# Performance work log

Measured on AMD Instinct MI355X. Metric: run time of the kernel, lower is better.

Reference implementation:

```python
import jax, jax.numpy as jnp
import numpy as np

D_MODEL = 2048
N_HEADS = 16
D_HEAD = D_MODEL // N_HEADS  # 128
T_MAX = 2048
B, T = 2, 2048


def _build_rope_cache(T_max, d_head):
    pos = jnp.arange(T_max, dtype=jnp.float32)[:, None]
    dim = jnp.arange(0, d_head, 2, dtype=jnp.float32)
    freqs = 1.0 / (10000.0 ** (dim / d_head))
    angles = pos * freqs  # [T_max, d_head//2]
    return jnp.cos(angles), jnp.sin(angles)


def _apply_rope(x, cos, sin):
    # x: [B, H, T, D]; cos/sin: [T_max, D//2]
    d2 = x.shape[-1] // 2
    x1, x2 = x[..., :d2], x[..., d2:]
    c = cos[: x.shape[2]][None, None]  # [1,1,T,D//2]
    s = sin[: x.shape[2]][None, None]
    return jnp.concatenate([x1 * c - x2 * s, x2 * c + x1 * s], axis=-1)


def setup_inputs() -> dict:
    key = jax.random.key(0)
    k1, k2, k3, k4 = jax.random.split(key, 4)
    x = jax.random.normal(k1, (B, T, D_MODEL), dtype=jnp.float32)
    Wqkv = jax.random.normal(k2, (3 * D_MODEL, D_MODEL), dtype=jnp.float32) * (D_MODEL ** -0.5)
    Wproj = jax.random.normal(k3, (D_MODEL, D_MODEL), dtype=jnp.float32) * (D_MODEL ** -0.5)
    q_gain = jnp.full((N_HEADS,), 1.0, dtype=jnp.float32) + 0.1 * jax.random.normal(k4, (N_HEADS,), dtype=jnp.float32)
    rope_cos, rope_sin = _build_rope_cache(T_MAX, D_HEAD)
    return {"x": x, "Wqkv": Wqkv, "Wproj": Wproj, "q_gain": q_gain,
            "rope_cos": rope_cos, "rope_sin": rope_sin}


def reference(x, Wqkv, Wproj, q_gain, rope_cos, rope_sin):
    Bx, Tx, C = x.shape
    H, D = N_HEADS, C // N_HEADS
    qkv = jnp.einsum('btc,fc->btf', x, Wqkv)  # [B,T,3C]
    q, k, v = jnp.split(qkv, 3, axis=2)
    q = q.reshape(Bx, Tx, H, D).transpose(0, 2, 1, 3)  # [B,H,T,D]
    k = k.reshape(Bx, Tx, H, D).transpose(0, 2, 1, 3)
    v = v.reshape(Bx, Tx, H, D).transpose(0, 2, 1, 3)
    q = _apply_rope(q, rope_cos, rope_sin)
    k = _apply_rope(k, rope_cos, rope_sin)
    q = q * q_gain[None, :, None, None]
    scale = 1.0 / jnp.sqrt(jnp.asarray(D, dtype=x.dtype))
    scores = jnp.einsum('bhqd,bhkd->bhqk', q, k) * scale
    causal = jnp.tril(jnp.ones((Tx, Tx), dtype=bool))
    scores = jnp.where(causal[None, None], scores, jnp.asarray(-jnp.inf, dtype=scores.dtype))
    attn = jax.nn.softmax(scores, axis=-1)
    y = jnp.einsum('bhqk,bhkd->bhqd', attn, v)  # [B,H,T,D]
    y = y.transpose(0, 2, 1, 3).reshape(Bx, Tx, C)
    return jnp.einsum('btc,oc->bto', y, Wproj)
```

## Files before the change

kernel.cpp:

```cpp
#include <hip/hip_runtime.h>
#include <stdint.h>

#define BB    2
#define T_SEQ 2048
#define NH    16
#define DH    128
#define DM    2048

typedef unsigned short u16;
typedef unsigned int   u32;
typedef __attribute__((ext_vector_type(8))) short short8;
typedef __attribute__((ext_vector_type(4))) short short4_t;
typedef __attribute__((ext_vector_type(4))) float floatx4;

__device__ __forceinline__ float bf2f(u16 b) { return __uint_as_float(((u32)b) << 16); }
__device__ __forceinline__ u16 f2bf(float f) {
    u32 u = __float_as_uint(f);
    u32 r = u + 0x7fffu + ((u >> 16) & 1u);
    return (u16)(r >> 16);
}

__device__ __forceinline__ short8 cvt8(const float* p) {
    floatx4 a = *(const floatx4*)p;
    floatx4 b = *(const floatx4*)(p + 4);
    short8 r;
    r[0] = (short)f2bf(a[0]); r[1] = (short)f2bf(a[1]);
    r[2] = (short)f2bf(a[2]); r[3] = (short)f2bf(a[3]);
    r[4] = (short)f2bf(b[0]); r[5] = (short)f2bf(b[1]);
    r[6] = (short)f2bf(b[2]); r[7] = (short)f2bf(b[3]);
    return r;
}

__device__ __forceinline__ void gl2lds16(const u16* g, u16* l) {
    __builtin_amdgcn_global_load_lds(
        (const __attribute__((address_space(1))) void*)g,
        (__attribute__((address_space(3))) void*)l, 16, 0, 0);
}

__global__ void detect_dtype(const u16* __restrict__ w, int* __restrict__ flag) {
    __shared__ int cnt;
    if (threadIdx.x == 0) cnt = 0;
    __syncthreads();
    int c = 0;
    for (int i = threadIdx.x; i < 2048; i += 256) {
        float v = bf2f(w[i]);
        if (!(fabsf(v) <= 1.0f)) c++;
    }
    atomicAdd(&cnt, c);
    __syncthreads();
    if (threadIdx.x == 0) *flag = (cnt > 64) ? 1 : 0;
}

__global__ void sentinel_k(const int* __restrict__ flag, float* __restrict__ out, int n) {
    if (*flag != 0) return;
    for (int i = threadIdx.x; i < n; i += 256) out[i] = (i == 0) ? 200.0f : 0.0f;
}

__global__ void fill_const(float* __restrict__ out, int n, float v0) {
    int i = blockIdx.x * 256 + threadIdx.x;
    if (i < n) out[i] = (i == 0) ? v0 : 0.0f;
}

__global__ __launch_bounds__(256) void cvt_f32_bf16(const float* __restrict__ src,
                                                    u16* __restrict__ dst, int n4,
                                                    const int* __restrict__ flag) {
    if (*flag == 0) return;
    int i = blockIdx.x * 256 + threadIdx.x;
    if (i < n4) {
        floatx4 v = ((const floatx4*)src)[i];
        short4_t r;
        r[0] = (short)f2bf(v[0]); r[1] = (short)f2bf(v[1]);
        r[2] = (short)f2bf(v[2]); r[3] = (short)f2bf(v[3]);
        ((short4_t*)dst)[i] = r;
    }
}

template<int PERM, int OF32>
__global__ __launch_bounds__(256) void gemm97(const u16* __restrict__ A,
                                              const u16* __restrict__ B,
                                              void* __restrict__ Cv,
                                              const int* __restrict__ flag,
                                              int M, int N, int K)
{
    if (*flag == 0) return;

    __shared__ __align__(16) u16 As[128 * 32];
    __shared__ __align__(16) u16 Bs[128 * 32];

    u16*   C16 = (u16*)Cv;
    float* C32 = (float*)Cv;

    const int tid  = threadIdx.x;
    const int lane = tid & 63;
    const int quad = lane >> 4;
    const int l15  = lane & 15;
    const int wave = tid >> 6;
    const int wy   = (wave >> 1) * 64;
    const int wx   = (wave & 1) * 64;
    const int rowA0 = blockIdx.y * 128;
    const int rowB0 = blockIdx.x * 128;

    const int lrow = lane >> 2;
    const int lcol = (lane & 3) << 3;
    const int segA0 = wave * 2, segA1 = wave * 2 + 1;

    const u16* gA0 = A + (size_t)(rowA0 + segA0 * 16 + lrow) * K + lcol;
    const u16* gA1 = A + (size_t)(rowA0 + segA1 * 16 + lrow) * K + lcol;
    const u16* gB0 = B + (size_t)(rowB0 + segA0 * 16 + lrow) * K + lcol;
    const u16* gB1 = B + (size_t)(rowB0 + segA1 * 16 + lrow) * K + lcol;
    u16* lA0 = &As[segA0 * 16 * 32];
    u16* lA1 = &As[segA1 * 16 * 32];
    u16* lB0 = &Bs[segA0 * 16 * 32];
    u16* lB1 = &Bs[segA1 * 16 * 32];

    floatx4 acc[4][4];
#pragma unroll
    for (int i = 0; i < 4; ++i)
#pragma unroll
        for (int j = 0; j < 4; ++j) acc[i][j] = (floatx4){0.f, 0.f, 0.f, 0.f};

    for (int k0 = 0; k0 < K; k0 += 32) {
        __syncthreads();
        gl2lds16(gA0 + k0, lA0);
        gl2lds16(gA1 + k0, lA1);
        gl2lds16(gB0 + k0, lB0);
        gl2lds16(gB1 + k0, lB1);
        __syncthreads();

        short8 a[4], b[4];
#pragma unroll
        for (int i = 0; i < 4; ++i)
            a[i] = *(const short8*)&As[(wy + i * 16 + l15) * 32 + quad * 8];
#pragma unroll
        for (int i = 0; i < 4; ++i)
            b[i] = *(const short8*)&Bs[(wx + i * 16 + l15) * 32 + quad * 8];
#pragma unroll
        for (int i = 0; i < 4; ++i)
#pragma unroll
            for (int j = 0; j < 4; ++j)
                acc[i][j] = __builtin_amdgcn_mfma_f32_16x16x32_bf16(a[i], b[j], acc[i][j], 0, 0, 0);
    }

#pragma unroll
    for (int i = 0; i < 4; ++i) {
#pragma unroll
        for (int j = 0; j < 4; ++j) {
#pragma unroll
            for (int r = 0; r < 4; ++r) {
                int row = rowA0 + wy + i * 16 + quad * 4 + r;
                int col = rowB0 + wx + j * 16 + l15;
                if (PERM == 3) {
                    int slice = rowB0 >> 11;
                    u16* dbuf = C16 + (size_t)slice * 8388608;
                    int b_ = row >> 11, t_ = row & 2047;
                    int colm = col & 2047;
                    int h_ = colm >> 7, d_ = colm & 127;
                    size_t dst;
                    if (slice < 2) {
                        dst = ((size_t)((b_ * NH + h_) * T_SEQ + t_)) * DH + d_;
                    } else {
                        int u  = t_ & 63;
                        int tp = (t_ & ~63) + ((u & 15) * 4) + (u >> 4);
                        dst = ((size_t)((b_ * NH + h_) * DH + d_)) * T_SEQ + tp;
                    }
                    dbuf[dst] = f2bf(acc[i][j][r]);
                } else {
                    size_t dst = (size_t)row * N + col;
                    if (OF32) C32[dst] = acc[i][j][r];
                    else      C16[dst] = f2bf(acc[i][j][r]);
                }
            }
        }
    }
}

template<int PERM, int AF32, int BF32, int OF32>
__global__ __launch_bounds__(256) void gemm_bt(const void* __restrict__ Av,
                                               const void* __restrict__ Bv,
                                               void* __restrict__ Cv,
                                               const int* __restrict__ flag,
                                               int bslice, int M, int N, int K)
{
    if (*flag == 0) return;

    __shared__ __align__(16) u16 As[128 * 32];
    __shared__ __align__(16) u16 Bs[128 * 32];

    const u16*   A16 = (const u16*)Av;
    const float* A32 = (const float*)Av;
    const u16*   B16 = (const u16*)Bv   + (size_t)bslice * DM * DM;
    const float* B32 = (const float*)Bv + (size_t)bslice * DM * DM;
    u16*   C16 = (u16*)Cv;
    float* C32 = (float*)Cv;

    const int tid  = threadIdx.x;
    const int lane = tid & 63;
    const int quad = lane >> 4;
    const int l15  = lane & 15;
    const int wave = tid >> 6;
    const int wy   = (wave >> 1) * 64;
    const int wx   = (wave & 1) * 64;
    const int rowA0 = blockIdx.y * 128;
    const int rowB0 = blockIdx.x * 128;

    const int srow = tid >> 2;
    const int scol = (tid & 3) << 3;

    const size_t aoff0 = (size_t)(rowA0 + srow) * K + scol;
    const size_t aoff1 = aoff0 + (size_t)64 * K;
    const size_t boff0 = (size_t)(rowB0 + srow) * K + scol;
    const size_t boff1 = boff0 + (size_t)64 * K;

    u16* AsW0 = &As[srow * 32 + scol];
    u16* AsW1 = &As[(srow + 64) * 32 + scol];
    u16* BsW0 = &Bs[srow * 32 + scol];
    u16* BsW1 = &Bs[(srow + 64) * 32 + scol];

    floatx4 acc[4][4];
#pragma unroll
    for (int i = 0; i < 4; ++i)
#pragma unroll
        for (int j = 0; j < 4; ++j) acc[i][j] = (floatx4){0.f, 0.f, 0.f, 0.f};

    for (int k0 = 0; k0 < K; k0 += 32) {
        short8 av0 = AF32 ? cvt8(A32 + aoff0 + k0) : *(const short8*)(A16 + aoff0 + k0);
        short8 av1 = AF32 ? cvt8(A32 + aoff1 + k0) : *(const short8*)(A16 + aoff1 + k0);
        short8 bv0 = BF32 ? cvt8(B32 + boff0 + k0) : *(const short8*)(B16 + boff0 + k0);
        short8 bv1 = BF32 ? cvt8(B32 + boff1 + k0) : *(const short8*)(B16 + boff1 + k0);
        __syncthreads();
        *(short8*)AsW0 = av0;
        *(short8*)AsW1 = av1;
        *(short8*)BsW0 = bv0;
        *(short8*)BsW1 = bv1;
        __syncthreads();

        short8 a[4], b[4];
#pragma unroll
        for (int i = 0; i < 4; ++i)
            a[i] = *(const short8*)&As[(wy + i * 16 + l15) * 32 + quad * 8];
#pragma unroll
        for (int i = 0; i < 4; ++i)
            b[i] = *(const short8*)&Bs[(wx + i * 16 + l15) * 32 + quad * 8];
#pragma unroll
        for (int i = 0; i < 4; ++i)
#pragma unroll
            for (int j = 0; j < 4; ++j)
                acc[i][j] = __builtin_amdgcn_mfma_f32_16x16x32_bf16(a[i], b[j], acc[i][j], 0, 0, 0);
    }

#pragma unroll
    for (int i = 0; i < 4; ++i) {
#pragma unroll
        for (int j = 0; j < 4; ++j) {
#pragma unroll
            for (int r = 0; r < 4; ++r) {
                int row = rowA0 + wy + i * 16 + quad * 4 + r;
                int col = rowB0 + wx + j * 16 + l15;
                size_t dst;
                if (PERM == 1) {
                    int b_ = row >> 11, t_ = row & 2047;
                    int h_ = col >> 7,  d_ = col & 127;
                    dst = ((size_t)((b_ * NH + h_) * T_SEQ + t_)) * DH + d_;
                } else if (PERM == 2) {
                    int b_ = row >> 11, t_ = row & 2047;
                    int h_ = col >> 7,  d_ = col & 127;
                    int u  = t_ & 63;
                    int tp = (t_ & ~63) + ((u & 15) * 4) + (u >> 4);
                    dst = ((size_t)((b_ * NH + h_) * DH + d_)) * T_SEQ + tp;
                } else {
                    dst = (size_t)row * N + col;
                }
                if (OF32) C32[dst] = acc[i][j][r];
                else      C16[dst] = f2bf(acc[i][j][r]);
            }
        }
    }
}

__global__ __launch_bounds__(256) void rope_inplace(u16* __restrict__ q,
                                                    u16* __restrict__ k,
                                                    const void* __restrict__ gainv,
                                                    const void* __restrict__ cosv,
                                                    const void* __restrict__ sinv,
                                                    const int* __restrict__ flag)
{
    if (*flag == 0) return;
    const float* gain = (const float*)gainv;
    const float* cosb = (const float*)cosv;
    const float* sinb = (const float*)sinv;

    int idx = blockIdx.x * 256 + threadIdx.x;
    int d2 = idx & 63;
    int t  = (idx >> 6) & 2047;
    int h  = (idx >> 17) & 15;
    int b  = idx >> 21;

    float c = cosb[t * 64 + d2];
    float s = sinb[t * 64 + d2];
    float g = gain[h] * 0.08838834764831843f * 1.4426950408889634f;

    size_t row = ((size_t)((b * NH + h) * T_SEQ + t)) * DH;
    float q1 = bf2f(q[row + d2]);
    float q2 = bf2f(q[row + 64 + d2]);
    q[row + d2]      = f2bf((q1 * c - q2 * s) * g);
    q[row + 64 + d2] = f2bf((q2 * c + q1 * s) * g);

    float k1 = bf2f(k[row + d2]);
    float k2 = bf2f(k[row + 64 + d2]);
    k[row + d2]      = f2bf(k1 * c - k2 * s);
    k[row + 64 + d2] = f2bf(k2 * c + k1 * s);
}

__global__ __launch_bounds__(256) void attn_flash3(const u16* __restrict__ q,
                                                   const u16* __restrict__ k,
                                                   const u16* __restrict__ v,
                                                   u16* __restrict__ y,
                                                   const int* __restrict__ flag)
{
    if (*flag == 0) return;

    __shared__ __align__(16) u16 Ks[64 * 128];
    __shared__ __align__(16) u16 Vt[128 * 64];
    __shared__ __align__(16) u16 Ps[4][16 * 64];

    const int tid  = threadIdx.x;
    const int lane = tid & 63;
    const int l15  = lane & 15;
    const int quad = lane >> 4;
    const int wave = tid >> 6;
    const int bh   = blockIdx.y;
    const int p    = blockIdx.x;

    const u16* kbase = k + (size_t)bh * T_SEQ * DH;
    const u16* vbase = v + (size_t)bh * DH * T_SEQ;
    const int b_ = bh >> 4, h_ = bh & 15;

    const int skey = tid >> 2;
    const int sg4  = (tid & 3) * 4;
    const int vdim = tid >> 1;
    const int vg4  = (tid & 1) * 4;

#define LOADKV(KT, KR, VR) do {                                               \
        const u16* kg_ = kbase + ((size_t)((KT) * 64 + skey)) * DH + sg4 * 8; \
        const u16* vg_ = vbase + (size_t)vdim * T_SEQ + (KT) * 64 + vg4 * 8;  \
        _Pragma("unroll")                                                     \
        for (int i_ = 0; i_ < 4; ++i_) KR[i_] = *(const short8*)(kg_ + i_ * 8); \
        _Pragma("unroll")                                                     \
        for (int i_ = 0; i_ < 4; ++i_) VR[i_] = *(const short8*)(vg_ + i_ * 8); \
    } while (0)

    for (int phase = 0; phase < 2; ++phase) {
        const int qt  = phase ? p : (T_SEQ / 64 - 1 - p);
        const int q0w = qt * 64 + wave * 16;
        const int iters = qt + 1;

        short8 aq[4];
        {
            const u16* qrow = q + ((size_t)bh * T_SEQ + q0w + l15) * DH + quad * 8;
#pragma unroll
            for (int s = 0; s < 4; ++s) aq[s] = *(const short8*)(qrow + s * 32);
        }

        floatx4 o[8];
#pragma unroll
        for (int n = 0; n < 8; ++n) o[n] = (floatx4){0.f, 0.f, 0.f, 0.f};
        float M = -1e30f;
        float l_r[4] = {0.f, 0.f, 0.f, 0.f};

        short8 krA[4], vrA[4], krB[4], vrB[4];
        LOADKV(0, krA, vrA);

        for (int kt = 0; kt < iters; ++kt) {
            __syncthreads();
#pragma unroll
            for (int i = 0; i < 4; ++i)
                *(short8*)&Ks[skey * 128 + (((sg4 + i) ^ (skey & 7)) << 3)] = krA[i];
#pragma unroll
            for (int i = 0; i < 4; ++i)
                *(short8*)&Vt[vdim * 64 + (((vg4 + i) ^ (vdim & 7)) << 3)] = vrA[i];
            __syncthreads();

            if (kt + 1 < iters) LOADKV(kt + 1, krB, vrB);

            floatx4 sc[4];
#pragma unroll
            for (int t = 0; t < 4; ++t) {
                sc[t] = (floatx4){0.f, 0.f, 0.f, 0.f};
#pragma unroll
                for (int s = 0; s < 4; ++s) {
                    short8 bk = *(const short8*)&Ks[(t * 16 + l15) * 128 +
                                                    (((s * 4 + quad) ^ (l15 & 7)) << 3)];
                    sc[t] = __builtin_amdgcn_mfma_f32_16x16x32_bf16(aq[s], bk, sc[t], 0, 0, 0);
                }
            }

            if (kt == qt) {
#pragma unroll
                for (int t = 0; t < 4; ++t)
#pragma unroll
                    for (int r = 0; r < 4; ++r)
                        if (kt * 64 + t * 16 + l15 > q0w + quad * 4 + r)
                            sc[t][r] = -1e30f;
            }
            float mloc = sc[0][0];
#pragma unroll
            for (int t = 0; t < 4; ++t)
#pragma unroll
                for (int r = 0; r < 4; ++r) mloc = fmaxf(mloc, sc[t][r]);
            mloc = fmaxf(mloc, __shfl_xor(mloc, 1));
            mloc = fmaxf(mloc, __shfl_xor(mloc, 2));
            mloc = fmaxf(mloc, __shfl_xor(mloc, 4));
            mloc = fmaxf(mloc, __shfl_xor(mloc, 8));
            mloc = fmaxf(mloc, __shfl_xor(mloc, 16));
            mloc = fmaxf(mloc, __shfl_xor(mloc, 32));
            float Mn = fmaxf(M, mloc);
            float al = exp2f(M - Mn);
            M = Mn;

            if (__builtin_amdgcn_readfirstlane(__float_as_uint(al)) != 0x3f800000u) {
#pragma unroll
                for (int n = 0; n < 8; ++n)
#pragma unroll
                    for (int r = 0; r < 4; ++r) o[n][r] *= al;
#pragma unroll
                for (int r = 0; r < 4; ++r) l_r[r] *= al;
            }

#pragma unroll
            for (int r = 0; r < 4; ++r) {
                float p0 = exp2f(sc[0][r] - M);
                float p1 = exp2f(sc[1][r] - M);
                float p2 = exp2f(sc[2][r] - M);
                float p3 = exp2f(sc[3][r] - M);
                float rs = p0 + p1 + p2 + p3;
                rs += __shfl_xor(rs, 1);
                rs += __shfl_xor(rs, 2);
                rs += __shfl_xor(rs, 4);
                rs += __shfl_xor(rs, 8);
                l_r[r] += rs;

                int qr = quad * 4 + r;
                u32 lo = (u32)f2bf(p0) | ((u32)f2bf(p1) << 16);
                u32 hi = (u32)f2bf(p2) | ((u32)f2bf(p3) << 16);
                u32* dst = (u32*)&Ps[wave][qr * 64 +
                                           (((l15 >> 1) ^ (qr & 7)) << 3) + (l15 & 1) * 4];
                dst[0] = lo;
                dst[1] = hi;
            }

#pragma unroll
            for (int s = 0; s < 2; ++s) {
                short8 ap = *(const short8*)&Ps[wave][l15 * 64 +
                                                      (((s * 4 + quad) ^ (l15 & 7)) << 3)];
#pragma unroll
                for (int n = 0; n < 8; ++n) {
                    short8 bv = *(const short8*)&Vt[(n * 16 + l15) * 64 +
                                                    (((s * 4 + quad) ^ (l15 & 7)) << 3)];
                    o[n] = __builtin_amdgcn_mfma_f32_16x16x32_bf16(ap, bv, o[n], 0, 0, 0);
                }
            }

#pragma unroll
            for (int i = 0; i < 4; ++i) { krA[i] = krB[i]; vrA[i] = vrB[i]; }
        }

#pragma unroll
        for (int r = 0; r < 4; ++r) {
            float inv = 1.f / l_r[r];
            int qrow = q0w + quad * 4 + r;
            size_t yo = ((size_t)(b_ * T_SEQ + qrow)) * DM + h_ * DH + l15;
#pragma unroll
            for (int n = 0; n < 8; ++n)
                y[yo + n * 16] = f2bf(o[n][r] * inv);
        }
    }
#undef LOADKV
}

extern "C" void kernel_launch(void* const* d_in, const int* in_sizes, int n_in,
                              void* d_out, int out_size, void* d_ws, size_t ws_size,
                              hipStream_t stream)
{
    float* out = (float*)d_out;
    const int FILLB = (out_size + 255) / 256;

    bool ok = (n_in == 6) &&
              in_sizes[0] == 8388608 && in_sizes[1] == 12582912 &&
              in_sizes[2] == 4194304 && in_sizes[3] == 16 &&
              in_sizes[4] == 131072  && in_sizes[5] == 131072 &&
              out_size == 8388608;
    if (!ok) {
        fill_const<<<FILLB, 256, 0, stream>>>(out, out_size, 150.0f);
        return;
    }

    const size_t MB = 1024 * 1024;
    const size_t BUF = 16 * MB;
    if (ws_size < 4 * BUF + 256) {
        fill_const<<<FILLB, 256, 0, stream>>>(out, out_size, 100.0f);
        return;
    }

    const void* x     = d_in[0];
    const void* Wqkv  = d_in[1];
    const void* Wproj = d_in[2];
    const void* qgain = d_in[3];
    const void* rc    = d_in[4];
    const void* rs    = d_in[5];

    char* ws = (char*)d_ws;
    const size_t FAST_NEED = 96 * MB + 256;

    if (ws_size >= FAST_NEED) {
        u16* qb   = (u16*)(ws);
        u16* kb   = (u16*)(ws + BUF);
        u16* vb   = (u16*)(ws + 2 * BUF);
        u16* wqbf = (u16*)(ws + 3 * BUF);
        u16* wpbf = (u16*)(ws + 3 * BUF + 24 * MB);
        u16* xbf  = (u16*)(ws + 5 * BUF);
        u16* yb   = xbf;
        int* flag = (int*)(ws + 6 * BUF);

        detect_dtype<<<1, 256, 0, stream>>>((const u16*)Wqkv, flag);

        cvt_f32_bf16<<<(8388608 / 4 + 255) / 256, 256, 0, stream>>>((const float*)x, xbf, 8388608 / 4, flag);
        cvt_f32_bf16<<<(12582912 / 4 + 255) / 256, 256, 0, stream>>>((const float*)Wqkv, wqbf, 12582912 / 4, flag);
        cvt_f32_bf16<<<(4194304 / 4 + 255) / 256, 256, 0, stream>>>((const float*)Wproj, wpbf, 4194304 / 4, flag);

        gemm97<3, 0><<<dim3(48, 32), 256, 0, stream>>>(xbf, wqbf, qb, flag, 4096, 6144, 2048);
        rope_inplace<<<16384, 256, 0, stream>>>(qb, kb, qgain, rc, rs, flag);
        attn_flash3<<<dim3(T_SEQ / 128, BB * NH), 256, 0, stream>>>(qb, kb, vb, yb, flag);
        gemm97<0, 1><<<dim3(16, 32), 256, 0, stream>>>(yb, wpbf, out, flag, 4096, 2048, 2048);
        sentinel_k<<<1, 256, 0, stream>>>(flag, out, out_size);
    } else {
        u16* qb = (u16*)(ws);
        u16* kb = (u16*)(ws + BUF);
        u16* vb = (u16*)(ws + 2 * BUF);
        u16* yb = (u16*)(ws + 3 * BUF);
        int* flag = (int*)(ws + 4 * BUF);

        detect_dtype<<<1, 256, 0, stream>>>((const u16*)Wqkv, flag);
        gemm_bt<1, 1, 1, 0><<<dim3(16, 32), 256, 0, stream>>>(x, Wqkv, qb, flag, 0, 4096, 2048, 2048);
        gemm_bt<1, 1, 1, 0><<<dim3(16, 32), 256, 0, stream>>>(x, Wqkv, kb, flag, 1, 4096, 2048, 2048);
        gemm_bt<2, 1, 1, 0><<<dim3(16, 32), 256, 0, stream>>>(x, Wqkv, vb, flag, 2, 4096, 2048, 2048);
        rope_inplace<<<16384, 256, 0, stream>>>(qb, kb, qgain, rc, rs, flag);
        attn_flash3<<<dim3(T_SEQ / 128, BB * NH), 256, 0, stream>>>(qb, kb, vb, yb, flag);
        gemm_bt<0, 0, 1, 1><<<dim3(16, 32), 256, 0, stream>>>(yb, Wproj, out, flag, 0, 4096, 2048, 2048);
        sentinel_k<<<1, 256, 0, stream>>>(flag, out, out_size);
    }
}
```

Measured before the change: 525.9 us.

## Launch one block per query tile and coalesce K/V tile loads

The attention kernel now handles a single 64-row query tile per block, with heaviest tiles scheduled first, instead of pairing a long and a short tile in one block across two phases. This doubles the grid to 1024 blocks, so the CUs can be filled better and the causal load balance is left to the hardware scheduler. K and V global loads are remapped so adjacent threads read adjacent 16-byte segments of a row, which improves coalescing. The trade-off is more blocks with uneven work and a repeated Q/prologue setup per block.

```diff
diff --git a/kernel.cpp b/kernel.cpp
--- a/kernel.cpp
+++ b/kernel.cpp
@@ -311,7 +311,7 @@
     k[row + 64 + d2] = f2bf(k2 * c + k1 * s);
 }
 
-__global__ __launch_bounds__(256) void attn_flash3(const u16* __restrict__ q,
+__global__ __launch_bounds__(256) void attn_flash4(const u16* __restrict__ q,
                                                    const u16* __restrict__ k,
                                                    const u16* __restrict__ v,
                                                    u16* __restrict__ y,
@@ -329,150 +329,152 @@
     const int quad = lane >> 4;
     const int wave = tid >> 6;
     const int bh   = blockIdx.y;
-    const int p    = blockIdx.x;
+    const int qt   = (T_SEQ / 64 - 1) - blockIdx.x;
 
     const u16* kbase = k + (size_t)bh * T_SEQ * DH;
     const u16* vbase = v + (size_t)bh * DH * T_SEQ;
     const int b_ = bh >> 4, h_ = bh & 15;
 
-    const int skey = tid >> 2;
-    const int sg4  = (tid & 3) * 4;
-    const int vdim = tid >> 1;
-    const int vg4  = (tid & 1) * 4;
+    const int krow = tid >> 4;
+    const int kseg = tid & 15;
+    const int vrow = tid >> 3;
+    const int vseg = tid & 7;
 
 #define LOADKV(KT, KR, VR) do {                                               \
-        const u16* kg_ = kbase + ((size_t)((KT) * 64 + skey)) * DH + sg4 * 8; \
-        const u16* vg_ = vbase + (size_t)vdim * T_SEQ + (KT) * 64 + vg4 * 8;  \
         _Pragma("unroll")                                                     \
-        for (int i_ = 0; i_ < 4; ++i_) KR[i_] = *(const short8*)(kg_ + i_ * 8); \
-        _Pragma("unroll")                                                     \
-        for (int i_ = 0; i_ < 4; ++i_) VR[i_] = *(const short8*)(vg_ + i_ * 8); \
+        for (int rg_ = 0; rg_ < 4; ++rg_) {                                   \
+            KR[rg_] = *(const short8*)(kbase +                                \
+                (size_t)((KT) * 64 + rg_ * 16 + krow) * DH + kseg * 8);       \
+            VR[rg_] = *(const short8*)(vbase +                                \
+                (size_t)(rg_ * 32 + vrow) * T_SEQ + (KT) * 64 + vseg * 8);    \
+        }                                                                     \
     } while (0)
 
-    for (int phase = 0; phase < 2; ++phase) {
-        const int qt  = phase ? p : (T_SEQ / 64 - 1 - p);
-        const int q0w = qt * 64 + wave * 16;
-        const int iters = qt + 1;
-
-        short8 aq[4];
-        {
-            const u16* qrow = q + ((size_t)bh * T_SEQ + q0w + l15) * DH + quad * 8;
-#pragma unroll
-            for (int s = 0; s < 4; ++s) aq[s] = *(const short8*)(qrow + s * 32);
-        }
-
-        floatx4 o[8];
-#pragma unroll
-        for (int n = 0; n < 8; ++n) o[n] = (floatx4){0.f, 0.f, 0.f, 0.f};
-        float M = -1e30f;
-        float l_r[4] = {0.f, 0.f, 0.f, 0.f};
-
-        short8 krA[4], vrA[4], krB[4], vrB[4];
-        LOADKV(0, krA, vrA);
-
-        for (int kt = 0; kt < iters; ++kt) {
-            __syncthreads();
-#pragma unroll
-            for (int i = 0; i < 4; ++i)
-                *(short8*)&Ks[skey * 128 + (((sg4 + i) ^ (skey & 7)) << 3)] = krA[i];
-#pragma unroll
-            for (int i = 0; i < 4; ++i)
-                *(short8*)&Vt[vdim * 64 + (((vg4 + i) ^ (vdim & 7)) << 3)] = vrA[i];
-            __syncthreads();
-
-            if (kt + 1 < iters) LOADKV(kt + 1, krB, vrB);
-
-            floatx4 sc[4];
-#pragma unroll
-            for (int t = 0; t < 4; ++t) {
-                sc[t] = (floatx4){0.f, 0.f, 0.f, 0.f};
-#pragma unroll
-                for (int s = 0; s < 4; ++s) {
-                    short8 bk = *(const short8*)&Ks[(t * 16 + l15) * 128 +
-                                                    (((s * 4 + quad) ^ (l15 & 7)) << 3)];
-                    sc[t] = __builtin_amdgcn_mfma_f32_16x16x32_bf16(aq[s], bk, sc[t], 0, 0, 0);
-                }
+    const int q0w = qt * 64 + wave * 16;
+    const int iters = qt + 1;
+
+    short8 aq[4];
+    {
+        const u16* qrow = q + ((size_t)bh * T_SEQ + q0w + l15) * DH + quad * 8;
+#pragma unroll
+        for (int s = 0; s < 4; ++s) aq[s] = *(const short8*)(qrow + s * 32);
+    }
+
+    floatx4 o[8];
+#pragma unroll
+    for (int n = 0; n < 8; ++n) o[n] = (floatx4){0.f, 0.f, 0.f, 0.f};
+    float M = -1e30f;
+    float l_r[4] = {0.f, 0.f, 0.f, 0.f};
+
+    short8 krA[4], vrA[4], krB[4], vrB[4];
+    LOADKV(0, krA, vrA);
+
+    for (int kt = 0; kt < iters; ++kt) {
+        __syncthreads();
+#pragma unroll
+        for (int rg_ = 0; rg_ < 4; ++rg_) {
+            int kr_ = rg_ * 16 + krow;
+            *(short8*)&Ks[kr_ * 128 + ((kseg ^ (kr_ & 7)) << 3)] = krA[rg_];
+        }
+#pragma unroll
+        for (int rg_ = 0; rg_ < 4; ++rg_) {
+            int vr_ = rg_ * 32 + vrow;
+            *(short8*)&Vt[vr_ * 64 + ((vseg ^ (vr_ & 7)) << 3)] = vrA[rg_];
+        }
+        __syncthreads();
+
+        if (kt + 1 < iters) LOADKV(kt + 1, krB, vrB);
+
+        floatx4 sc[4];
+#pragma unroll
+        for (int t = 0; t < 4; ++t) {
+            sc[t] = (floatx4){0.f, 0.f, 0.f, 0.f};
+#pragma unroll
+            for (int s = 0; s < 4; ++s) {
+                short8 bk = *(const short8*)&Ks[(t * 16 + l15) * 128 +
+                                                (((s * 4 + quad) ^ (l15 & 7)) << 3)];
+                sc[t] = __builtin_amdgcn_mfma_f32_16x16x32_bf16(aq[s], bk, sc[t], 0, 0, 0);
             }
-
-            if (kt == qt) {
-#pragma unroll
-                for (int t = 0; t < 4; ++t)
-#pragma unroll
-                    for (int r = 0; r < 4; ++r)
-                        if (kt * 64 + t * 16 + l15 > q0w + quad * 4 + r)
-                            sc[t][r] = -1e30f;
+        }
+
+        if (kt == qt) {
+#pragma unroll
+            for (int t = 0; t < 4; ++t)
+#pragma unroll
+                for (int r = 0; r < 4; ++r)
+                    if (kt * 64 + t * 16 + l15 > q0w + quad * 4 + r)
+                        sc[t][r] = -1e30f;
+        }
+        float mloc = sc[0][0];
+#pragma unroll
+        for (int t = 0; t < 4; ++t)
+#pragma unroll
+            for (int r = 0; r < 4; ++r) mloc = fmaxf(mloc, sc[t][r]);
+        mloc = fmaxf(mloc, __shfl_xor(mloc, 1));
+        mloc = fmaxf(mloc, __shfl_xor(mloc, 2));
+        mloc = fmaxf(mloc, __shfl_xor(mloc, 4));
+        mloc = fmaxf(mloc, __shfl_xor(mloc, 8));
+        mloc = fmaxf(mloc, __shfl_xor(mloc, 16));
+        mloc = fmaxf(mloc, __shfl_xor(mloc, 32));
+        float Mn = fmaxf(M, mloc);
+        float al = exp2f(M - Mn);
+        M = Mn;
+
+        if (__builtin_amdgcn_readfirstlane(__float_as_uint(al)) != 0x3f800000u) {
+#pragma unroll
+            for (int n = 0; n < 8; ++n)
+#pragma unroll
+                for (int r = 0; r < 4; ++r) o[n][r] *= al;
+#pragma unroll
+            for (int r = 0; r < 4; ++r) l_r[r] *= al;
+        }
+
+#pragma unroll
+        for (int r = 0; r < 4; ++r) {
+            float p0 = exp2f(sc[0][r] - M);
+            float p1 = exp2f(sc[1][r] - M);
+            float p2 = exp2f(sc[2][r] - M);
+            float p3 = exp2f(sc[3][r] - M);
+            float rs = p0 + p1 + p2 + p3;
+            rs += __shfl_xor(rs, 1);
+            rs += __shfl_xor(rs, 2);
+            rs += __shfl_xor(rs, 4);
+            rs += __shfl_xor(rs, 8);
+            l_r[r] += rs;
+
+            int qr = quad * 4 + r;
+            u32 lo = (u32)f2bf(p0) | ((u32)f2bf(p1) << 16);
+            u32 hi = (u32)f2bf(p2) | ((u32)f2bf(p3) << 16);
+            u32* dst = (u32*)&Ps[wave][qr * 64 +
+                                       (((l15 >> 1) ^ (qr & 7)) << 3) + (l15 & 1) * 4];
+            dst[0] = lo;
+            dst[1] = hi;
+        }
+
+#pragma unroll
+        for (int s = 0; s < 2; ++s) {
+            short8 ap = *(const short8*)&Ps[wave][l15 * 64 +
+                                                  (((s * 4 + quad) ^ (l15 & 7)) << 3)];
+#pragma unroll
+            for (int n = 0; n < 8; ++n) {
+                short8 bv = *(const short8*)&Vt[(n * 16 + l15) * 64 +
+                                                (((s * 4 + quad) ^ (l15 & 7)) << 3)];
+                o[n] = __builtin_amdgcn_mfma_f32_16x16x32_bf16(ap, bv, o[n], 0, 0, 0);
             }
-            float mloc = sc[0][0];
-#pragma unroll
-            for (int t = 0; t < 4; ++t)
-#pragma unroll
-                for (int r = 0; r < 4; ++r) mloc = fmaxf(mloc, sc[t][r]);
-            mloc = fmaxf(mloc, __shfl_xor(mloc, 1));
-            mloc = fmaxf(mloc, __shfl_xor(mloc, 2));
-            mloc = fmaxf(mloc, __shfl_xor(mloc, 4));
-            mloc = fmaxf(mloc, __shfl_xor(mloc, 8));
-            mloc = fmaxf(mloc, __shfl_xor(mloc, 16));
-            mloc = fmaxf(mloc, __shfl_xor(mloc, 32));
-            float Mn = fmaxf(M, mloc);
-            float al = exp2f(M - Mn);
-            M = Mn;
-
-            if (__builtin_amdgcn_readfirstlane(__float_as_uint(al)) != 0x3f800000u) {
-#pragma unroll
-                for (int n = 0; n < 8; ++n)
-#pragma unroll
-                    for (int r = 0; r < 4; ++r) o[n][r] *= al;
-#pragma unroll
-                for (int r = 0; r < 4; ++r) l_r[r] *= al;
-            }
-
-#pragma unroll
-            for (int r = 0; r < 4; ++r) {
-                float p0 = exp2f(sc[0][r] - M);
-                float p1 = exp2f(sc[1][r] - M);
-                float p2 = exp2f(sc[2][r] - M);
-                float p3 = exp2f(sc[3][r] - M);
-                float rs = p0 + p1 + p2 + p3;
-                rs += __shfl_xor(rs, 1);
-                rs += __shfl_xor(rs, 2);
-                rs += __shfl_xor(rs, 4);
-                rs += __shfl_xor(rs, 8);
-                l_r[r] += rs;
-
-                int qr = quad * 4 + r;
-                u32 lo = (u32)f2bf(p0) | ((u32)f2bf(p1) << 16);
-                u32 hi = (u32)f2bf(p2) | ((u32)f2bf(p3) << 16);
-                u32* dst = (u32*)&Ps[wave][qr * 64 +
-                                           (((l15 >> 1) ^ (qr & 7)) << 3) + (l15 & 1) * 4];
-                dst[0] = lo;
-                dst[1] = hi;
-            }
-
-#pragma unroll
-            for (int s = 0; s < 2; ++s) {
-                short8 ap = *(const short8*)&Ps[wave][l15 * 64 +
-                                                      (((s * 4 + quad) ^ (l15 & 7)) << 3)];
-#pragma unroll
-                for (int n = 0; n < 8; ++n) {
-                    short8 bv = *(const short8*)&Vt[(n * 16 + l15) * 64 +
-                                                    (((s * 4 + quad) ^ (l15 & 7)) << 3)];
-                    o[n] = __builtin_amdgcn_mfma_f32_16x16x32_bf16(ap, bv, o[n], 0, 0, 0);
-                }
-            }
-
-#pragma unroll
-            for (int i = 0; i < 4; ++i) { krA[i] = krB[i]; vrA[i] = vrB[i]; }
-        }
-
-#pragma unroll
-        for (int r = 0; r < 4; ++r) {
-            float inv = 1.f / l_r[r];
-            int qrow = q0w + quad * 4 + r;
-            size_t yo = ((size_t)(b_ * T_SEQ + qrow)) * DM + h_ * DH + l15;
-#pragma unroll
-            for (int n = 0; n < 8; ++n)
-                y[yo + n * 16] = f2bf(o[n][r] * inv);
-        }
+        }
+
+#pragma unroll
+        for (int i = 0; i < 4; ++i) { krA[i] = krB[i]; vrA[i] = vrB[i]; }
+    }
+
+#pragma unroll
+    for (int r = 0; r < 4; ++r) {
+        float inv = 1.f / l_r[r];
+        int qrow = q0w + quad * 4 + r;
+        size_t yo = ((size_t)(b_ * T_SEQ + qrow)) * DM + h_ * DH + l15;
+#pragma unroll
+        for (int n = 0; n < 8; ++n)
+            y[yo + n * 16] = f2bf(o[n][r] * inv);
     }
 #undef LOADKV
 }
@@ -529,7 +531,7 @@
 
         gemm97<3, 0><<<dim3(48, 32), 256, 0, stream>>>(xbf, wqbf, qb, flag, 4096, 6144, 2048);
         rope_inplace<<<16384, 256, 0, stream>>>(qb, kb, qgain, rc, rs, flag);
-        attn_flash3<<<dim3(T_SEQ / 128, BB * NH), 256, 0, stream>>>(qb, kb, vb, yb, flag);
+        attn_flash4<<<dim3(T_SEQ / 64, BB * NH), 256, 0, stream>>>(qb, kb, vb, yb, flag);
         gemm97<0, 1><<<dim3(16, 32), 256, 0, stream>>>(yb, wpbf, out, flag, 4096, 2048, 2048);
         sentinel_k<<<1, 256, 0, stream>>>(flag, out, out_size);
     } else {
@@ -544,7 +546,7 @@
         gemm_bt<1, 1, 1, 0><<<dim3(16, 32), 256, 0, stream>>>(x, Wqkv, kb, flag, 1, 4096, 2048, 2048);
         gemm_bt<2, 1, 1, 0><<<dim3(16, 32), 256, 0, stream>>>(x, Wqkv, vb, flag, 2, 4096, 2048, 2048);
         rope_inplace<<<16384, 256, 0, stream>>>(qb, kb, qgain, rc, rs, flag);
-        attn_flash3<<<dim3(T_SEQ / 128, BB * NH), 256, 0, stream>>>(qb, kb, vb, yb, flag);
+        attn_flash4<<<dim3(T_SEQ / 64, BB * NH), 256, 0, stream>>>(qb, kb, vb, yb, flag);
         gemm_bt<0, 0, 1, 1><<<dim3(16, 32), 256, 0, stream>>>(yb, Wproj, out, flag, 0, 4096, 2048, 2048);
         sentinel_k<<<1, 256, 0, stream>>>(flag, out, out_size);
     }
```

Measured after the change: 531.7 us. About the same (+1.1%).
